# Performance work log

Measured on AMD Instinct MI355X. Metric: run time of the kernel, lower is better.

The kernel has to match this reference:

```python
import jax, jax.numpy as jnp
import numpy as np

B, M, T, N = 128, 256, 512, 512

def setup_inputs() -> dict:
    key = jax.random.key(0)
    ks = jax.random.split(key, 6)
    return {
        "hidden_state": jax.random.normal(ks[0], (B, M), jnp.float32),
        "cell_state": jax.random.normal(ks[1], (B, M), jnp.float32),
        "X": jax.random.normal(ks[2], (B, T, N), jnp.float32),
        "We1": jax.random.normal(ks[3], (2 * M, T), jnp.float32) * 0.05,
        "be1": jnp.zeros((T,), jnp.float32),
        "We2": jax.random.normal(ks[4], (T, T), jnp.float32) * 0.05,
        "be2": jnp.zeros((T,), jnp.float32),
        "v": jax.random.normal(ks[5], (T, 1), jnp.float32) * 0.05,
        "bv": jnp.zeros((1,), jnp.float32),
    }

def reference(hidden_state, cell_state, X, We1, be1, We2, be2, v, bv):
    # concat hidden + cell: [B, 2m]; Dense(T) then broadcast over n (K.repeat)
    hc = jnp.concatenate([hidden_state, cell_state], axis=-1)
    hs = (hc @ We1 + be1)[:, None, :]                 # [B, 1, T] (broadcast over n)
    # Permute X -> [B, n, T], Dense(T): contract over T
    ux = jnp.einsum('btn,tk->bnk', X, We2) + be2      # [B, n, T]
    # add + tanh + Dense(1) fused chain
    e = jnp.tanh(hs + ux) @ v + bv                    # [B, n, 1]
    # Permute -> [B, 1, n], softmax over last axis (n)
    attn = jax.nn.softmax(jnp.swapaxes(e, 1, 2), axis=-1)  # [B, 1, n]
    return attn
```

## Files before the change

kernel.cpp:

```cpp
#include <hip/hip_runtime.h>
#include <hip/hip_bf16.h>


typedef _Float16 half8 __attribute__((ext_vector_type(8)));
typedef float floatx4 __attribute__((ext_vector_type(4)));

#define GLOAD_LDS16(gp, lp) __builtin_amdgcn_global_load_lds(                  \
    (const __attribute__((address_space(1))) void*)(const void*)(gp),          \
    (__attribute__((address_space(3))) void*)(void*)(lp), 16, 0, 0)

__device__ __forceinline__ float fast_tanh(float x) {
    float cx = fminf(15.0f, fmaxf(-15.0f, x));
    float e = __expf(2.0f * cx);
    return (e - 1.0f) * __fdividef(1.0f, e + 1.0f);
}

__global__ __launch_bounds__(256) void k_prep_a(const float* __restrict__ We2,
                                                _Float16* __restrict__ Af) {
    __shared__ float w2[32][512];
    const int ts = blockIdx.x;
    for (int idx = threadIdx.x; idx < 32 * 512; idx += 256) {
        int tl = idx >> 9, k = idx & 511;
        w2[tl][k] = We2[(ts * 32 + tl) * 512 + k];
    }
    __syncthreads();
    for (int item = threadIdx.x; item < 32 * 64; item += 256) {
        int c = item >> 6, l = item & 63;
        int k  = c * 16 + (l & 15);
        int tl = (l >> 4) * 8;
        half8 h;
#pragma unroll
        for (int j = 0; j < 8; ++j) h[j] = (_Float16)w2[tl + j][k];
        *(half8*)&Af[(((size_t)ts * 32 + c) * 64 + l) * 8] = h;
    }
}

__global__ __launch_bounds__(256) void k_hs(const float* __restrict__ hidden,
                                            const float* __restrict__ cell,
                                            const float* __restrict__ We1,
                                            const float* __restrict__ be1,
                                            const float* __restrict__ be2,
                                            float* __restrict__ g) {
    __shared__ __align__(16) float hcl[8][512];
    __shared__ float red[4][8][64];
    const int b0 = (blockIdx.x >> 3) << 3;
    const int k0 = (blockIdx.x & 7) << 6;
    for (int idx = threadIdx.x; idx < 8 * 512; idx += 256) {
        int bi = idx >> 9, j = idx & 511;
        hcl[bi][j] = (j < 256) ? hidden[(b0 + bi) * 256 + j]
                               : cell[(b0 + bi) * 256 + j - 256];
    }
    __syncthreads();
    const int kl = threadIdx.x & 63;
    const int jc = threadIdx.x >> 6;
    const int k  = k0 + kl;
    float acc[8] = {};
    for (int j = jc * 128; j < jc * 128 + 128; j += 4) {
        float w0 = We1[(j + 0) * 512 + k];
        float w1 = We1[(j + 1) * 512 + k];
        float w2 = We1[(j + 2) * 512 + k];
        float w3 = We1[(j + 3) * 512 + k];
#pragma unroll
        for (int bi = 0; bi < 8; ++bi) {
            float4 h = *(const float4*)&hcl[bi][j];
            acc[bi] += h.x * w0 + h.y * w1 + h.z * w2 + h.w * w3;
        }
    }
#pragma unroll
    for (int bi = 0; bi < 8; ++bi) red[jc][bi][kl] = acc[bi];
    __syncthreads();
    for (int idx = threadIdx.x; idx < 512; idx += 256) {
        int bi = idx >> 6, kk = idx & 63;
        float s = red[0][bi][kk] + red[1][bi][kk] + red[2][bi][kk] + red[3][bi][kk];
        int kg = k0 + kk;
        g[(b0 + bi) * 512 + kg] = s + be1[kg] + be2[kg];
    }
}

__global__ __launch_bounds__(512, 4) void k_main(const float* __restrict__ X,
                                                 const _Float16* __restrict__ Af,
                                                 const float* __restrict__ g,
                                                 const float* __restrict__ vvec,
                                                 float* __restrict__ E) {
    __shared__ __align__(16) _Float16 Ab[2][16384];
    __shared__ __align__(16) _Float16 Xb[2][2048];
    const int b    = blockIdx.x >> 3;
    const int n0   = (blockIdx.x & 7) << 6;
    const int tid  = threadIdx.x;
    const int lane = tid & 63;
    const int wv   = tid >> 6;
    const int l16  = lane & 15;
    const int lhi  = lane >> 4;

    const float* Xg = X + (size_t)b * (512 * 512) + n0;
    const int  xn    = tid & 63;
    const int  xo    = (tid >> 6) & 3;
    const bool xact  = (tid < 256);
    const int  xslot = ((xn >> 4) * 64 + xo * 16 + (xn & 15)) * 8;
    const _Float16* AgW = Af + (size_t)wv * 2048 + (size_t)lane * 8;

    {
#pragma unroll
        for (int i = 0; i < 4; ++i)
            GLOAD_LDS16(AgW + i * 512, &Ab[0][wv * 2048 + i * 512 + lane * 8]);
        if (xact) {
            float f[8];
#pragma unroll
            for (int j = 0; j < 8; ++j) f[j] = Xg[(size_t)(xo * 8 + j) * 512 + xn];
            half8 h;
#pragma unroll
            for (int j = 0; j < 8; ++j) h[j] = (_Float16)f[j];
            *(half8*)&Xb[0][xslot] = h;
        }
    }
    __syncthreads();

    floatx4 acc[4][4];
#pragma unroll
    for (int a = 0; a < 4; ++a)
#pragma unroll
        for (int c = 0; c < 4; ++c) acc[a][c] = (floatx4){0.f, 0.f, 0.f, 0.f};

    float xf[8];
    for (int ts = 0; ts < 16; ++ts) {
        const int cur = ts & 1;
        const int nxt = cur ^ 1;
        if (ts < 15) {
#pragma unroll
            for (int i = 0; i < 4; ++i)
                GLOAD_LDS16(AgW + (size_t)(ts + 1) * 16384 + i * 512,
                            &Ab[nxt][wv * 2048 + i * 512 + lane * 8]);
            if (xact) {
#pragma unroll
                for (int j = 0; j < 8; ++j)
                    xf[j] = Xg[(size_t)((ts + 1) * 32 + xo * 8 + j) * 512 + xn];
            }
        }
        {
            half8 af0 = *(const half8*)&Ab[cur][(wv * 4 + 0) * 512 + lane * 8];
            half8 af1 = *(const half8*)&Ab[cur][(wv * 4 + 1) * 512 + lane * 8];
            half8 af2 = *(const half8*)&Ab[cur][(wv * 4 + 2) * 512 + lane * 8];
            half8 af3 = *(const half8*)&Ab[cur][(wv * 4 + 3) * 512 + lane * 8];
#pragma unroll
            for (int nf = 0; nf < 4; ++nf) {
                half8 bf = *(const half8*)&Xb[cur][(nf * 64 + lane) * 8];
                acc[0][nf] = __builtin_amdgcn_mfma_f32_16x16x32_f16(af0, bf, acc[0][nf], 0, 0, 0);
                acc[1][nf] = __builtin_amdgcn_mfma_f32_16x16x32_f16(af1, bf, acc[1][nf], 0, 0, 0);
                acc[2][nf] = __builtin_amdgcn_mfma_f32_16x16x32_f16(af2, bf, acc[2][nf], 0, 0, 0);
                acc[3][nf] = __builtin_amdgcn_mfma_f32_16x16x32_f16(af3, bf, acc[3][nf], 0, 0, 0);
            }
        }
        if (ts < 15 && xact) {
            half8 h;
#pragma unroll
            for (int j = 0; j < 8; ++j) h[j] = (_Float16)xf[j];
            *(half8*)&Xb[nxt][xslot] = h;
        }
        __syncthreads();
    }

    const float* gb = g + b * 512;
    float s[4] = {0.f, 0.f, 0.f, 0.f};
#pragma unroll
    for (int kf = 0; kf < 4; ++kf) {
        const int kb = wv * 64 + kf * 16 + lhi * 4;
        float g0 = gb[kb + 0], g1 = gb[kb + 1], g2 = gb[kb + 2], g3 = gb[kb + 3];
        float v0 = vvec[kb + 0], v1 = vvec[kb + 1], v2 = vvec[kb + 2], v3 = vvec[kb + 3];
#pragma unroll
        for (int nf = 0; nf < 4; ++nf) {
            s[nf] += fast_tanh(acc[kf][nf][0] + g0) * v0;
            s[nf] += fast_tanh(acc[kf][nf][1] + g1) * v1;
            s[nf] += fast_tanh(acc[kf][nf][2] + g2) * v2;
            s[nf] += fast_tanh(acc[kf][nf][3] + g3) * v3;
        }
    }
#pragma unroll
    for (int nf = 0; nf < 4; ++nf) {
        s[nf] += __shfl_xor(s[nf], 16);
        s[nf] += __shfl_xor(s[nf], 32);
    }
    __syncthreads();
    float* ered = (float*)&Ab[0][0];
    if (lane < 16) {
#pragma unroll
        for (int nf = 0; nf < 4; ++nf) ered[wv * 64 + nf * 16 + l16] = s[nf];
    }
    __syncthreads();
    if (tid < 64) {
        float e = 0.f;
#pragma unroll
        for (int w = 0; w < 8; ++w) e += ered[w * 64 + tid];
        E[b * 512 + n0 + tid] = e;
    }
}

__global__ __launch_bounds__(256) void k_softmax(const float* __restrict__ E,
                                                 float* __restrict__ out) {
    __shared__ float rmax[4], rsum[4];
    const int b = blockIdx.x;
    const int tid = threadIdx.x;
    float e0 = E[b * 512 + tid];
    float e1 = E[b * 512 + 256 + tid];
    float m = fmaxf(e0, e1);
    for (int o = 32; o > 0; o >>= 1) m = fmaxf(m, __shfl_xor(m, o));
    if ((tid & 63) == 0) rmax[tid >> 6] = m;
    __syncthreads();
    m = fmaxf(fmaxf(rmax[0], rmax[1]), fmaxf(rmax[2], rmax[3]));
    float p0 = __expf(e0 - m), p1 = __expf(e1 - m);
    float ss = p0 + p1;
    for (int o = 32; o > 0; o >>= 1) ss += __shfl_xor(ss, o);
    if ((tid & 63) == 0) rsum[tid >> 6] = ss;
    __syncthreads();
    ss = rsum[0] + rsum[1] + rsum[2] + rsum[3];
    float inv = __fdividef(1.0f, ss);
    out[b * 512 + tid] = p0 * inv;
    out[b * 512 + 256 + tid] = p1 * inv;
}

extern "C" void kernel_launch(void* const* d_in, const int* in_sizes, int n_in,
                              void* d_out, int out_size, void* d_ws, size_t ws_size,
                              hipStream_t stream) {
    const float* hidden = (const float*)d_in[0];
    const float* cell   = (const float*)d_in[1];
    const float* X      = (const float*)d_in[2];
    const float* We1    = (const float*)d_in[3];
    const float* be1    = (const float*)d_in[4];
    const float* We2    = (const float*)d_in[5];
    const float* be2    = (const float*)d_in[6];
    const float* v      = (const float*)d_in[7];
    float* out = (float*)d_out;

    char* ws = (char*)d_ws;
    _Float16* Af = (_Float16*)ws;
    float* g     = (float*)(ws + 524288);
    float* E     = (float*)(ws + 524288 + 262144);

    k_prep_a<<<16, 256, 0, stream>>>(We2, Af);
    k_hs<<<128, 256, 0, stream>>>(hidden, cell, We1, be1, be2, g);
    k_main<<<1024, 512, 0, stream>>>(X, Af, g, v, E);
    k_softmax<<<128, 256, 0, stream>>>(E, out);
}
```

Measured before the change: 83.01 us.

## Spread X loads over all waves with two-stage register prefetch and manual waitcnt barriers

The X tile load is now split across all eight waves (four rows each, half4 LDS stores) rather than only the first four waves. X is prefetched two k-steps ahead into alternating register sets. The full __syncthreads is replaced by explicit s_waitcnt vmcnt(4) plus s_barrier so that the outstanding X global loads need not drain each iteration. MFMA sections are also wrapped in s_setprio, and the loop is fully unrolled. This aims to hide global latency for X and reduce barrier stalls, but the hand-written vmcnt counts must exactly match the issued loads, and full unrolling raises register pressure.

```diff
diff --git a/kernel.cpp b/kernel.cpp
--- a/kernel.cpp
+++ b/kernel.cpp
@@ -3,6 +3,7 @@
 
 
 typedef _Float16 half8 __attribute__((ext_vector_type(8)));
+typedef _Float16 half4 __attribute__((ext_vector_type(4)));
 typedef float floatx4 __attribute__((ext_vector_type(4)));
 
 #define GLOAD_LDS16(gp, lp) __builtin_amdgcn_global_load_lds(                  \
@@ -93,27 +94,31 @@
     const int lhi  = lane >> 4;
 
     const float* Xg = X + (size_t)b * (512 * 512) + n0;
-    const int  xn    = tid & 63;
-    const int  xo    = (tid >> 6) & 3;
-    const bool xact  = (tid < 256);
-    const int  xslot = ((xn >> 4) * 64 + xo * 16 + (xn & 15)) * 8;
+    const int xn = lane;
+    const int xslot = ((xn >> 4) * 64 + (wv >> 1) * 16 + (xn & 15)) * 8 + (wv & 1) * 4;
     const _Float16* AgW = Af + (size_t)wv * 2048 + (size_t)lane * 8;
 
+    float xrA[4], xrB[4];
+
+#pragma unroll
+    for (int i = 0; i < 4; ++i)
+        GLOAD_LDS16(AgW + i * 512, &Ab[0][wv * 2048 + i * 512 + lane * 8]);
+#pragma unroll
+    for (int j = 0; j < 4; ++j)
+        xrA[j] = Xg[(size_t)(wv * 4 + j) * 512 + xn];
+#pragma unroll
+    for (int j = 0; j < 4; ++j)
+        xrB[j] = Xg[(size_t)(32 + wv * 4 + j) * 512 + xn];
     {
-#pragma unroll
-        for (int i = 0; i < 4; ++i)
-            GLOAD_LDS16(AgW + i * 512, &Ab[0][wv * 2048 + i * 512 + lane * 8]);
-        if (xact) {
-            float f[8];
-#pragma unroll
-            for (int j = 0; j < 8; ++j) f[j] = Xg[(size_t)(xo * 8 + j) * 512 + xn];
-            half8 h;
-#pragma unroll
-            for (int j = 0; j < 8; ++j) h[j] = (_Float16)f[j];
-            *(half8*)&Xb[0][xslot] = h;
-        }
-    }
-    __syncthreads();
+        half4 h;
+#pragma unroll
+        for (int j = 0; j < 4; ++j) h[j] = (_Float16)xrA[j];
+        *(half4*)&Xb[0][xslot] = h;
+    }
+    asm volatile("s_waitcnt vmcnt(4) lgkmcnt(0)" ::: "memory");
+    __builtin_amdgcn_sched_barrier(0);
+    __builtin_amdgcn_s_barrier();
+    __builtin_amdgcn_sched_barrier(0);
 
     floatx4 acc[4][4];
 #pragma unroll
@@ -121,7 +126,7 @@
 #pragma unroll
         for (int c = 0; c < 4; ++c) acc[a][c] = (floatx4){0.f, 0.f, 0.f, 0.f};
 
-    float xf[8];
+#pragma unroll
     for (int ts = 0; ts < 16; ++ts) {
         const int cur = ts & 1;
         const int nxt = cur ^ 1;
@@ -130,17 +135,35 @@
             for (int i = 0; i < 4; ++i)
                 GLOAD_LDS16(AgW + (size_t)(ts + 1) * 16384 + i * 512,
                             &Ab[nxt][wv * 2048 + i * 512 + lane * 8]);
-            if (xact) {
-#pragma unroll
-                for (int j = 0; j < 8; ++j)
-                    xf[j] = Xg[(size_t)((ts + 1) * 32 + xo * 8 + j) * 512 + xn];
-            }
+        }
+        if (ts < 14) {
+            if ((ts & 1) == 0) {
+#pragma unroll
+                for (int j = 0; j < 4; ++j)
+                    xrA[j] = Xg[(size_t)((ts + 2) * 32 + wv * 4 + j) * 512 + xn];
+            } else {
+#pragma unroll
+                for (int j = 0; j < 4; ++j)
+                    xrB[j] = Xg[(size_t)((ts + 2) * 32 + wv * 4 + j) * 512 + xn];
+            }
+        }
+        if (ts < 15) {
+            half4 h;
+            if ((ts & 1) == 0) {
+#pragma unroll
+                for (int j = 0; j < 4; ++j) h[j] = (_Float16)xrB[j];
+            } else {
+#pragma unroll
+                for (int j = 0; j < 4; ++j) h[j] = (_Float16)xrA[j];
+            }
+            *(half4*)&Xb[nxt][xslot] = h;
         }
         {
             half8 af0 = *(const half8*)&Ab[cur][(wv * 4 + 0) * 512 + lane * 8];
             half8 af1 = *(const half8*)&Ab[cur][(wv * 4 + 1) * 512 + lane * 8];
             half8 af2 = *(const half8*)&Ab[cur][(wv * 4 + 2) * 512 + lane * 8];
             half8 af3 = *(const half8*)&Ab[cur][(wv * 4 + 3) * 512 + lane * 8];
+            __builtin_amdgcn_s_setprio(1);
 #pragma unroll
             for (int nf = 0; nf < 4; ++nf) {
                 half8 bf = *(const half8*)&Xb[cur][(nf * 64 + lane) * 8];
@@ -149,14 +172,18 @@
                 acc[2][nf] = __builtin_amdgcn_mfma_f32_16x16x32_f16(af2, bf, acc[2][nf], 0, 0, 0);
                 acc[3][nf] = __builtin_amdgcn_mfma_f32_16x16x32_f16(af3, bf, acc[3][nf], 0, 0, 0);
             }
-        }
-        if (ts < 15 && xact) {
-            half8 h;
-#pragma unroll
-            for (int j = 0; j < 8; ++j) h[j] = (_Float16)xf[j];
-            *(half8*)&Xb[nxt][xslot] = h;
-        }
-        __syncthreads();
+            __builtin_amdgcn_s_setprio(0);
+        }
+        if (ts < 15) {
+            if (ts < 14) {
+                asm volatile("s_waitcnt vmcnt(4) lgkmcnt(0)" ::: "memory");
+            } else {
+                asm volatile("s_waitcnt vmcnt(0) lgkmcnt(0)" ::: "memory");
+            }
+            __builtin_amdgcn_sched_barrier(0);
+            __builtin_amdgcn_s_barrier();
+            __builtin_amdgcn_sched_barrier(0);
+        }
     }
 
     const float* gb = g + b * 512;
```

Result: no change. 83.27 us (+0.3%).

## Split main GEMM over K-halves with triple-buffered A and staged X

Applied to the files above, without the earlier changes.

The main kernel now splits the 512 output features into two halves across separate 256-thread blocks, doubling the grid. Each block writes partial attention scores that the softmax kernel sums. A is loaded through a three-deep LDS ring with explicit vmcnt waits and raised MFMA priority. X is converted to fp16 and staged into LDS in two large chunks rather than per step. This aims to overlap global loads with MFMA work and remove per-iteration barriers. The cost is that every X tile is now read by two blocks, and the two half-loads of X stall compute.

```diff
diff --git a/kernel.cpp b/kernel.cpp
--- a/kernel.cpp
+++ b/kernel.cpp
@@ -77,15 +77,18 @@
     }
 }
 
-__global__ __launch_bounds__(512, 4) void k_main(const float* __restrict__ X,
+__global__ __launch_bounds__(256, 2) void k_main(const float* __restrict__ X,
                                                  const _Float16* __restrict__ Af,
                                                  const float* __restrict__ g,
                                                  const float* __restrict__ vvec,
-                                                 float* __restrict__ E) {
-    __shared__ __align__(16) _Float16 Ab[2][16384];
-    __shared__ __align__(16) _Float16 Xb[2][2048];
-    const int b    = blockIdx.x >> 3;
-    const int n0   = (blockIdx.x & 7) << 6;
+                                                 float* __restrict__ Ep) {
+    __shared__ __align__(16) _Float16 Ab[24576];
+    __shared__ __align__(16) _Float16 Xb[16384];
+    const int bid  = blockIdx.x;
+    const int ksl  = bid & 1;
+    const int nt   = (bid >> 1) & 7;
+    const int b    = bid >> 4;
+    const int n0   = nt << 6;
     const int tid  = threadIdx.x;
     const int lane = tid & 63;
     const int wv   = tid >> 6;
@@ -93,27 +96,46 @@
     const int lhi  = lane >> 4;
 
     const float* Xg = X + (size_t)b * (512 * 512) + n0;
-    const int  xn    = tid & 63;
-    const int  xo    = (tid >> 6) & 3;
-    const bool xact  = (tid < 256);
-    const int  xslot = ((xn >> 4) * 64 + xo * 16 + (xn & 15)) * 8;
-    const _Float16* AgW = Af + (size_t)wv * 2048 + (size_t)lane * 8;
-
-    {
-#pragma unroll
-        for (int i = 0; i < 4; ++i)
-            GLOAD_LDS16(AgW + i * 512, &Ab[0][wv * 2048 + i * 512 + lane * 8]);
-        if (xact) {
-            float f[8];
-#pragma unroll
-            for (int j = 0; j < 8; ++j) f[j] = Xg[(size_t)(xo * 8 + j) * 512 + xn];
-            half8 h;
-#pragma unroll
-            for (int j = 0; j < 8; ++j) h[j] = (_Float16)f[j];
-            *(half8*)&Xb[0][xslot] = h;
-        }
-    }
-    __syncthreads();
+    const _Float16* AgW = Af + (size_t)(ksl * 16 + wv * 4) * 512 + (size_t)lane * 8;
+    _Float16* AbW = &Ab[wv * 3 * 4 * 512 + lane * 8];
+
+#define ISSUE_A(ts, buf)                                                       \
+    {                                                                          \
+        _Pragma("unroll")                                                      \
+        for (int i = 0; i < 4; ++i)                                            \
+            GLOAD_LDS16(AgW + (size_t)(ts) * 16384 + i * 512,                  \
+                        AbW + (buf) * 2048 + i * 512);                         \
+    }
+
+    const int xn = lane;
+    const int xsl = ((xn >> 4) * 64 + wv * 16 + (xn & 15)) * 8;
+#define STAGE_X(p)                                                             \
+    {                                                                          \
+        _Pragma("unroll")                                                      \
+        for (int it = 0; it < 8; ++it) {                                       \
+            const int t0 = (p) * 256 + it * 32 + wv * 8;                       \
+            float f[8];                                                        \
+            _Pragma("unroll")                                                  \
+            for (int j = 0; j < 8; ++j) f[j] = Xg[(size_t)(t0 + j) * 512 + xn];\
+            half8 h;                                                           \
+            _Pragma("unroll")                                                  \
+            for (int j = 0; j < 8; ++j) h[j] = (_Float16)f[j];                 \
+            *(half8*)&Xb[it * 2048 + xsl] = h;                                 \
+        }                                                                      \
+    }
+
+#define LGKM_BARRIER()                                                         \
+    {                                                                          \
+        asm volatile("s_waitcnt lgkmcnt(0)" ::: "memory");                     \
+        __builtin_amdgcn_sched_barrier(0);                                     \
+        __builtin_amdgcn_s_barrier();                                          \
+        __builtin_amdgcn_sched_barrier(0);                                     \
+    }
+
+    ISSUE_A(0, 0);
+    ISSUE_A(1, 1);
+    STAGE_X(0);
+    LGKM_BARRIER();
 
     floatx4 acc[4][4];
 #pragma unroll
@@ -121,49 +143,48 @@
 #pragma unroll
         for (int c = 0; c < 4; ++c) acc[a][c] = (floatx4){0.f, 0.f, 0.f, 0.f};
 
-    float xf[8];
-    for (int ts = 0; ts < 16; ++ts) {
-        const int cur = ts & 1;
-        const int nxt = cur ^ 1;
-        if (ts < 15) {
-#pragma unroll
-            for (int i = 0; i < 4; ++i)
-                GLOAD_LDS16(AgW + (size_t)(ts + 1) * 16384 + i * 512,
-                            &Ab[nxt][wv * 2048 + i * 512 + lane * 8]);
-            if (xact) {
-#pragma unroll
-                for (int j = 0; j < 8; ++j)
-                    xf[j] = Xg[(size_t)((ts + 1) * 32 + xo * 8 + j) * 512 + xn];
-            }
-        }
-        {
-            half8 af0 = *(const half8*)&Ab[cur][(wv * 4 + 0) * 512 + lane * 8];
-            half8 af1 = *(const half8*)&Ab[cur][(wv * 4 + 1) * 512 + lane * 8];
-            half8 af2 = *(const half8*)&Ab[cur][(wv * 4 + 2) * 512 + lane * 8];
-            half8 af3 = *(const half8*)&Ab[cur][(wv * 4 + 3) * 512 + lane * 8];
-#pragma unroll
-            for (int nf = 0; nf < 4; ++nf) {
-                half8 bf = *(const half8*)&Xb[cur][(nf * 64 + lane) * 8];
-                acc[0][nf] = __builtin_amdgcn_mfma_f32_16x16x32_f16(af0, bf, acc[0][nf], 0, 0, 0);
-                acc[1][nf] = __builtin_amdgcn_mfma_f32_16x16x32_f16(af1, bf, acc[1][nf], 0, 0, 0);
-                acc[2][nf] = __builtin_amdgcn_mfma_f32_16x16x32_f16(af2, bf, acc[2][nf], 0, 0, 0);
-                acc[3][nf] = __builtin_amdgcn_mfma_f32_16x16x32_f16(af3, bf, acc[3][nf], 0, 0, 0);
-            }
-        }
-        if (ts < 15 && xact) {
-            half8 h;
-#pragma unroll
-            for (int j = 0; j < 8; ++j) h[j] = (_Float16)xf[j];
-            *(half8*)&Xb[nxt][xslot] = h;
-        }
-        __syncthreads();
-    }
+#define STEP(ts, lts)                                                          \
+    {                                                                          \
+        if ((ts) + 2 < 16) ISSUE_A((ts) + 2, ((ts) + 2) % 3);                  \
+        if ((ts) < 14)                                                         \
+            asm volatile("s_waitcnt vmcnt(8)" ::: "memory");                   \
+        else if ((ts) == 14)                                                   \
+            asm volatile("s_waitcnt vmcnt(4)" ::: "memory");                   \
+        else                                                                   \
+            asm volatile("s_waitcnt vmcnt(0)" ::: "memory");                   \
+        __builtin_amdgcn_sched_barrier(0);                                     \
+        const _Float16* ab = AbW + ((ts) % 3) * 2048;                          \
+        half8 af0 = *(const half8*)(ab);                                       \
+        half8 af1 = *(const half8*)(ab + 512);                                 \
+        half8 af2 = *(const half8*)(ab + 1024);                                \
+        half8 af3 = *(const half8*)(ab + 1536);                                \
+        __builtin_amdgcn_s_setprio(1);                                         \
+        _Pragma("unroll")                                                      \
+        for (int nf = 0; nf < 4; ++nf) {                                       \
+            half8 bf = *(const half8*)&Xb[((lts) * 4 + nf) * 512 + lane * 8];  \
+            acc[0][nf] = __builtin_amdgcn_mfma_f32_16x16x32_f16(af0, bf, acc[0][nf], 0, 0, 0); \
+            acc[1][nf] = __builtin_amdgcn_mfma_f32_16x16x32_f16(af1, bf, acc[1][nf], 0, 0, 0); \
+            acc[2][nf] = __builtin_amdgcn_mfma_f32_16x16x32_f16(af2, bf, acc[2][nf], 0, 0, 0); \
+            acc[3][nf] = __builtin_amdgcn_mfma_f32_16x16x32_f16(af3, bf, acc[3][nf], 0, 0, 0); \
+        }                                                                      \
+        __builtin_amdgcn_s_setprio(0);                                         \
+    }
+
+#pragma unroll
+    for (int lts = 0; lts < 8; ++lts) { STEP(lts, lts); }
+
+    LGKM_BARRIER();
+    STAGE_X(1);
+    LGKM_BARRIER();
+
+#pragma unroll
+    for (int lts = 0; lts < 8; ++lts) { STEP(8 + lts, lts); }
 
     const float* gb = g + b * 512;
     float s[4] = {0.f, 0.f, 0.f, 0.f};
 #pragma unroll
     for (int kf = 0; kf < 4; ++kf) {
-        const int kb = wv * 64 + kf * 16 + lhi * 4;
+        const int kb = ksl * 256 + wv * 64 + kf * 16 + lhi * 4;
         float g0 = gb[kb + 0], g1 = gb[kb + 1], g2 = gb[kb + 2], g3 = gb[kb + 3];
         float v0 = vvec[kb + 0], v1 = vvec[kb + 1], v2 = vvec[kb + 2], v3 = vvec[kb + 3];
 #pragma unroll
@@ -180,27 +201,31 @@
         s[nf] += __shfl_xor(s[nf], 32);
     }
     __syncthreads();
-    float* ered = (float*)&Ab[0][0];
+    float* ered = (float*)&Xb[0];
     if (lane < 16) {
 #pragma unroll
         for (int nf = 0; nf < 4; ++nf) ered[wv * 64 + nf * 16 + l16] = s[nf];
     }
     __syncthreads();
     if (tid < 64) {
-        float e = 0.f;
-#pragma unroll
-        for (int w = 0; w < 8; ++w) e += ered[w * 64 + tid];
-        E[b * 512 + n0 + tid] = e;
-    }
-}
-
-__global__ __launch_bounds__(256) void k_softmax(const float* __restrict__ E,
+        float e = ered[tid] + ered[64 + tid] + ered[128 + tid] + ered[192 + tid];
+        Ep[(size_t)ksl * (128 * 512) + b * 512 + n0 + tid] = e;
+    }
+#undef STEP
+#undef STAGE_X
+#undef ISSUE_A
+#undef LGKM_BARRIER
+}
+
+__global__ __launch_bounds__(256) void k_softmax(const float* __restrict__ Ep,
                                                  float* __restrict__ out) {
     __shared__ float rmax[4], rsum[4];
     const int b = blockIdx.x;
     const int tid = threadIdx.x;
-    float e0 = E[b * 512 + tid];
-    float e1 = E[b * 512 + 256 + tid];
+    const float* E0 = Ep;
+    const float* E1 = Ep + 128 * 512;
+    float e0 = E0[b * 512 + tid] + E1[b * 512 + tid];
+    float e1 = E0[b * 512 + 256 + tid] + E1[b * 512 + 256 + tid];
     float m = fmaxf(e0, e1);
     for (int o = 32; o > 0; o >>= 1) m = fmaxf(m, __shfl_xor(m, o));
     if ((tid & 63) == 0) rmax[tid >> 6] = m;
@@ -233,10 +258,10 @@
     char* ws = (char*)d_ws;
     _Float16* Af = (_Float16*)ws;
     float* g     = (float*)(ws + 524288);
-    float* E     = (float*)(ws + 524288 + 262144);
+    float* Ep    = (float*)(ws + 524288 + 262144);
 
     k_prep_a<<<16, 256, 0, stream>>>(We2, Af);
     k_hs<<<128, 256, 0, stream>>>(hidden, cell, We1, be1, be2, g);
-    k_main<<<1024, 512, 0, stream>>>(X, Af, g, v, E);
-    k_softmax<<<128, 256, 0, stream>>>(E, out);
-}
+    k_main<<<2048, 256, 0, stream>>>(X, Af, g, v, Ep);
+    k_softmax<<<128, 256, 0, stream>>>(Ep, out);
+}
```

Result: slower. 90.65 us (+9.2%).

## Split output-feature dimension across blocks and DMA fp32 X into triple-buffered LDS

Applied to the files above, without the earlier changes.

The main GEMM kernel now splits the 512 output features into two halves handled by separate 256-thread blocks, and writes two partial energy arrays that the softmax kernel sums. X is copied fp32 straight into a swizzled triple-buffered LDS ring with direct global-to-LDS loads and converted to fp16 when read. A weights are read directly from global/L2 instead of staged in LDS. Blocks are remapped so the X tiles of one batch are shared across neighbouring blocks, and the loop uses explicit waitcnt, barriers and setprio. The intent is to hide load latency and remove the register round trip for X, at the cost of each X tile being fetched by two blocks and partial tanh sums being written twice.

```diff
diff --git a/kernel.cpp b/kernel.cpp
--- a/kernel.cpp
+++ b/kernel.cpp
@@ -3,6 +3,7 @@
 
 
 typedef _Float16 half8 __attribute__((ext_vector_type(8)));
+typedef _Float16 half2v __attribute__((ext_vector_type(2)));
 typedef float floatx4 __attribute__((ext_vector_type(4)));
 
 #define GLOAD_LDS16(gp, lp) __builtin_amdgcn_global_load_lds(                  \
@@ -77,130 +78,138 @@
     }
 }
 
-__global__ __launch_bounds__(512, 4) void k_main(const float* __restrict__ X,
+__global__ __launch_bounds__(256, 3) void k_main(const float* __restrict__ X,
                                                  const _Float16* __restrict__ Af,
                                                  const float* __restrict__ g,
                                                  const float* __restrict__ vvec,
-                                                 float* __restrict__ E) {
-    __shared__ __align__(16) _Float16 Ab[2][16384];
-    __shared__ __align__(16) _Float16 Xb[2][2048];
-    const int b    = blockIdx.x >> 3;
-    const int n0   = (blockIdx.x & 7) << 6;
+                                                 float* __restrict__ Ep) {
+    __shared__ __align__(16) float Xs[3][4096];
     const int tid  = threadIdx.x;
     const int lane = tid & 63;
     const int wv   = tid >> 6;
     const int l16  = lane & 15;
     const int lhi  = lane >> 4;
-
-    const float* Xg = X + (size_t)b * (512 * 512) + n0;
-    const int  xn    = tid & 63;
-    const int  xo    = (tid >> 6) & 3;
-    const bool xact  = (tid < 256);
-    const int  xslot = ((xn >> 4) * 64 + xo * 16 + (xn & 15)) * 8;
-    const _Float16* AgW = Af + (size_t)wv * 2048 + (size_t)lane * 8;
-
-    {
-#pragma unroll
-        for (int i = 0; i < 4; ++i)
-            GLOAD_LDS16(AgW + i * 512, &Ab[0][wv * 2048 + i * 512 + lane * 8]);
-        if (xact) {
-            float f[8];
-#pragma unroll
-            for (int j = 0; j < 8; ++j) f[j] = Xg[(size_t)(xo * 8 + j) * 512 + xn];
-            half8 h;
-#pragma unroll
-            for (int j = 0; j < 8; ++j) h[j] = (_Float16)f[j];
-            *(half8*)&Xb[0][xslot] = h;
+    const int logical = ((blockIdx.x & 7) << 8) | (blockIdx.x >> 3);
+    const int kblk = logical & 1;
+    const int nt   = (logical >> 1) & 7;
+    const int b    = logical >> 4;
+    const int n0   = nt << 6;
+
+    const float* Xg = X + (size_t)b * 262144 + n0;
+    const _Float16* AgW = Af + (size_t)(kblk * 16 + wv * 4) * 512 + (size_t)lane * 8;
+
+    int xsrc[4], xdst[4];
+#pragma unroll
+    for (int p = 0; p < 4; ++p) {
+        int t_loc = (wv << 4) + (p << 2) + (lane >> 4);
+        int c_g   = (lane & 15) ^ (((t_loc >> 3) & 3) << 1);
+        xsrc[p] = t_loc * 512 + c_g * 4;
+        xdst[p] = ((wv << 4) + (p << 2)) * 64 + lane * 4;
+    }
+#define XDMA(s_, b_)                                                           \
+    { _Pragma("unroll")                                                        \
+      for (int p = 0; p < 4; ++p)                                              \
+          GLOAD_LDS16(Xg + (size_t)(s_) * 32768 + xsrc[p], &Xs[b_][xdst[p]]); }
+
+    const int q = l16 >> 2, r = l16 & 3;
+    int boff[4];
+#pragma unroll
+    for (int nf = 0; nf < 4; ++nf)
+        boff[nf] = lhi * 512 + ((((nf << 2) + q) ^ (lhi << 1)) << 2) + r;
+
+    XDMA(0, 0);
+    XDMA(1, 1);
+
+    floatx4 acc[4][4];
+#pragma unroll
+    for (int a = 0; a < 4; ++a)
+#pragma unroll
+        for (int c = 0; c < 4; ++c) acc[a][c] = (floatx4){0.f, 0.f, 0.f, 0.f};
+
+#pragma unroll
+    for (int s = 0; s < 8; ++s) {
+        const int buf = s % 3;
+        if (s < 7) asm volatile("s_waitcnt vmcnt(4)" ::: "memory");
+        else       asm volatile("s_waitcnt vmcnt(0)" ::: "memory");
+        asm volatile("s_waitcnt lgkmcnt(0)" ::: "memory");
+        __builtin_amdgcn_sched_barrier(0);
+        __builtin_amdgcn_s_barrier();
+        __builtin_amdgcn_sched_barrier(0);
+        if (s + 2 < 8) XDMA(s + 2, (s + 2) % 3);
+#pragma unroll
+        for (int ko = 0; ko < 2; ++ko) {
+            half8 af[4];
+#pragma unroll
+            for (int kf = 0; kf < 4; ++kf)
+                af[kf] = *(const half8*)
+                    (AgW + (size_t)(2 * s + ko) * 16384 + kf * 512);
+            half8 bf[4];
+#pragma unroll
+            for (int nf = 0; nf < 4; ++nf) {
+                union { half2v h2[4]; half8 h8; } u;
+#pragma unroll
+                for (int m = 0; m < 4; ++m) {
+                    float f0 = Xs[buf][boff[nf] + ko * 2048 + (2 * m) * 64];
+                    float f1 = Xs[buf][boff[nf] + ko * 2048 + (2 * m + 1) * 64];
+                    u.h2[m] = __builtin_bit_cast(half2v,
+                                  __builtin_amdgcn_cvt_pkrtz(f0, f1));
+                }
+                bf[nf] = u.h8;
+            }
+            __builtin_amdgcn_s_setprio(1);
+#pragma unroll
+            for (int kf = 0; kf < 4; ++kf)
+#pragma unroll
+                for (int nf = 0; nf < 4; ++nf)
+                    acc[kf][nf] = __builtin_amdgcn_mfma_f32_16x16x32_f16(
+                        af[kf], bf[nf], acc[kf][nf], 0, 0, 0);
+            __builtin_amdgcn_s_setprio(0);
         }
     }
-    __syncthreads();
-
-    floatx4 acc[4][4];
-#pragma unroll
-    for (int a = 0; a < 4; ++a)
-#pragma unroll
-        for (int c = 0; c < 4; ++c) acc[a][c] = (floatx4){0.f, 0.f, 0.f, 0.f};
-
-    float xf[8];
-    for (int ts = 0; ts < 16; ++ts) {
-        const int cur = ts & 1;
-        const int nxt = cur ^ 1;
-        if (ts < 15) {
-#pragma unroll
-            for (int i = 0; i < 4; ++i)
-                GLOAD_LDS16(AgW + (size_t)(ts + 1) * 16384 + i * 512,
-                            &Ab[nxt][wv * 2048 + i * 512 + lane * 8]);
-            if (xact) {
-#pragma unroll
-                for (int j = 0; j < 8; ++j)
-                    xf[j] = Xg[(size_t)((ts + 1) * 32 + xo * 8 + j) * 512 + xn];
-            }
-        }
-        {
-            half8 af0 = *(const half8*)&Ab[cur][(wv * 4 + 0) * 512 + lane * 8];
-            half8 af1 = *(const half8*)&Ab[cur][(wv * 4 + 1) * 512 + lane * 8];
-            half8 af2 = *(const half8*)&Ab[cur][(wv * 4 + 2) * 512 + lane * 8];
-            half8 af3 = *(const half8*)&Ab[cur][(wv * 4 + 3) * 512 + lane * 8];
-#pragma unroll
-            for (int nf = 0; nf < 4; ++nf) {
-                half8 bf = *(const half8*)&Xb[cur][(nf * 64 + lane) * 8];
-                acc[0][nf] = __builtin_amdgcn_mfma_f32_16x16x32_f16(af0, bf, acc[0][nf], 0, 0, 0);
-                acc[1][nf] = __builtin_amdgcn_mfma_f32_16x16x32_f16(af1, bf, acc[1][nf], 0, 0, 0);
-                acc[2][nf] = __builtin_amdgcn_mfma_f32_16x16x32_f16(af2, bf, acc[2][nf], 0, 0, 0);
-                acc[3][nf] = __builtin_amdgcn_mfma_f32_16x16x32_f16(af3, bf, acc[3][nf], 0, 0, 0);
-            }
-        }
-        if (ts < 15 && xact) {
-            half8 h;
-#pragma unroll
-            for (int j = 0; j < 8; ++j) h[j] = (_Float16)xf[j];
-            *(half8*)&Xb[nxt][xslot] = h;
-        }
-        __syncthreads();
-    }
+#undef XDMA
 
     const float* gb = g + b * 512;
-    float s[4] = {0.f, 0.f, 0.f, 0.f};
+    float sacc[4] = {0.f, 0.f, 0.f, 0.f};
 #pragma unroll
     for (int kf = 0; kf < 4; ++kf) {
-        const int kb = wv * 64 + kf * 16 + lhi * 4;
+        const int kb = kblk * 256 + wv * 64 + kf * 16 + lhi * 4;
         float g0 = gb[kb + 0], g1 = gb[kb + 1], g2 = gb[kb + 2], g3 = gb[kb + 3];
         float v0 = vvec[kb + 0], v1 = vvec[kb + 1], v2 = vvec[kb + 2], v3 = vvec[kb + 3];
 #pragma unroll
         for (int nf = 0; nf < 4; ++nf) {
-            s[nf] += fast_tanh(acc[kf][nf][0] + g0) * v0;
-            s[nf] += fast_tanh(acc[kf][nf][1] + g1) * v1;
-            s[nf] += fast_tanh(acc[kf][nf][2] + g2) * v2;
-            s[nf] += fast_tanh(acc[kf][nf][3] + g3) * v3;
+            sacc[nf] += fast_tanh(acc[kf][nf][0] + g0) * v0;
+            sacc[nf] += fast_tanh(acc[kf][nf][1] + g1) * v1;
+            sacc[nf] += fast_tanh(acc[kf][nf][2] + g2) * v2;
+            sacc[nf] += fast_tanh(acc[kf][nf][3] + g3) * v3;
         }
     }
 #pragma unroll
     for (int nf = 0; nf < 4; ++nf) {
-        s[nf] += __shfl_xor(s[nf], 16);
-        s[nf] += __shfl_xor(s[nf], 32);
-    }
-    __syncthreads();
-    float* ered = (float*)&Ab[0][0];
+        sacc[nf] += __shfl_xor(sacc[nf], 16);
+        sacc[nf] += __shfl_xor(sacc[nf], 32);
+    }
+    __syncthreads();
+    float* ered = (float*)&Xs[0][0];
     if (lane < 16) {
 #pragma unroll
-        for (int nf = 0; nf < 4; ++nf) ered[wv * 64 + nf * 16 + l16] = s[nf];
+        for (int nf = 0; nf < 4; ++nf) ered[wv * 64 + nf * 16 + l16] = sacc[nf];
     }
     __syncthreads();
     if (tid < 64) {
-        float e = 0.f;
-#pragma unroll
-        for (int w = 0; w < 8; ++w) e += ered[w * 64 + tid];
-        E[b * 512 + n0 + tid] = e;
-    }
-}
-
-__global__ __launch_bounds__(256) void k_softmax(const float* __restrict__ E,
+        float e = ered[tid] + ered[64 + tid] + ered[128 + tid] + ered[192 + tid];
+        Ep[(size_t)kblk * 65536 + b * 512 + n0 + tid] = e;
+    }
+}
+
+__global__ __launch_bounds__(256) void k_softmax(const float* __restrict__ Ep,
                                                  float* __restrict__ out) {
     __shared__ float rmax[4], rsum[4];
     const int b = blockIdx.x;
     const int tid = threadIdx.x;
-    float e0 = E[b * 512 + tid];
-    float e1 = E[b * 512 + 256 + tid];
+    const float* E0 = Ep;
+    const float* E1 = Ep + 65536;
+    float e0 = E0[b * 512 + tid] + E1[b * 512 + tid];
+    float e1 = E0[b * 512 + 256 + tid] + E1[b * 512 + 256 + tid];
     float m = fmaxf(e0, e1);
     for (int o = 32; o > 0; o >>= 1) m = fmaxf(m, __shfl_xor(m, o));
     if ((tid & 63) == 0) rmax[tid >> 6] = m;
@@ -233,10 +242,10 @@
     char* ws = (char*)d_ws;
     _Float16* Af = (_Float16*)ws;
     float* g     = (float*)(ws + 524288);
-    float* E     = (float*)(ws + 524288 + 262144);
+    float* Ep    = (float*)(ws + 786432);
 
     k_prep_a<<<16, 256, 0, stream>>>(We2, Af);
     k_hs<<<128, 256, 0, stream>>>(hidden, cell, We1, be1, be2, g);
-    k_main<<<1024, 512, 0, stream>>>(X, Af, g, v, E);
-    k_softmax<<<128, 256, 0, stream>>>(E, out);
-}
+    k_main<<<2048, 256, 0, stream>>>(X, Af, g, v, Ep);
+    k_softmax<<<128, 256, 0, stream>>>(Ep, out);
+}
```

Measured after the change: 83.23 us. No clear change (+0.3%).
